# Kernel tuning notes

Measured on AMD Instinct MI355X. Metric: run time of the kernel, lower is better.

Reference implementation:

```python
import jax, jax.numpy as jnp
import numpy as np

N, D, C = 16384, 1024, 1024
EPS = 1e-6       # F.pairwise_distance eps added to the difference
DENOM_EPS = 1e-5


def setup_inputs() -> dict:
    key = jax.random.key(0)
    k1, k2, k3 = jax.random.split(key, 3)
    features = jax.random.normal(k1, (N, D), dtype=jnp.float32)
    labels = jax.random.randint(k2, (N,), 0, 10, dtype=jnp.int64)
    centers = jax.random.normal(k3, (C, D), dtype=jnp.float32)
    return {"features": features, "labels": labels, "centers": centers}


def reference(features, labels, centers):
    # torch: dist = ||f - c + eps||_2 per (sample, center) pair.
    # Expand exactly: ||f - c + eps||^2 = ||f||^2 + ||c||^2 - 2 f.c
    #                 + 2*eps*(sum(f) - sum(c)) + eps^2 * D
    f2 = jnp.sum(features * features, axis=1)            # [N]
    c2 = jnp.sum(centers * centers, axis=1)              # [C]
    fc = features @ centers.T                            # [N, C]
    fs = jnp.sum(features, axis=1)                       # [N]
    cs = jnp.sum(centers, axis=1)                        # [C]
    d = features.shape[1]
    sq = (f2[:, None] + c2[None, :] - 2.0 * fc
          + 2.0 * EPS * (fs[:, None] - cs[None, :]) + (EPS * EPS) * d)
    dist = jnp.sqrt(jnp.maximum(sq, 0.0))                # [N, C]
    min_dist = jnp.min(dist, axis=1)                     # [N]
    mask = (labels == 0).astype(min_dist.dtype)          # select label==0 samples
    count = jnp.sum(mask)
    loss = jnp.sum(min_dist * mask) / (count + DENOM_EPS)
    return loss
```

## Files before the change

### kernel.cpp

```cpp
#include <hip/hip_runtime.h>


constexpr int N = 16384;
constexpr int D = 1024;
constexpr int C = 1024;
constexpr float EPS = 1e-6f;

constexpr int SB = 16;
constexpr int CB = 128;
constexpr int BK = 64;
constexpr int NKT = D / BK;
constexpr int TPB = 256;
constexpr int DIST_GRID = 1024;

typedef __attribute__((ext_vector_type(8))) short bf16x8;
typedef __attribute__((ext_vector_type(4))) float f32x4;

__device__ inline unsigned mapf(float f) {
  unsigned b = __float_as_uint(f);
  return (b & 0x80000000u) ? ~b : (b | 0x80000000u);
}
__device__ inline float unmapf(unsigned u) {
  return __uint_as_float((u & 0x80000000u) ? (u ^ 0x80000000u) : ~u);
}

__device__ inline unsigned short f2bf(float x) {
  unsigned u = __float_as_uint(x);
  return (unsigned short)((u + 0x7FFFu + ((u >> 16) & 1u)) >> 16);
}

#define GLOAD_LDS16(gp, lp)                                        \
  __builtin_amdgcn_global_load_lds(                                \
      (const __attribute__((address_space(1))) void*)(gp),         \
      (__attribute__((address_space(3))) void*)(lp), 16, 0, 0)

__global__ __launch_bounds__(TPB) void k_setup(
    const float* __restrict__ feat, const int* __restrict__ labels,
    const float* __restrict__ cent, unsigned* __restrict__ count,
    unsigned* __restrict__ sel, unsigned* __restrict__ minmapped,
    float* __restrict__ cc, float* __restrict__ ff,
    unsigned short* __restrict__ cent_bf) {
  __shared__ float red[8];
  __shared__ unsigned lrow[16], lslot[16];
  __shared__ int lcount;

  const int b = blockIdx.x, t = threadIdx.x;
  const int lane = t & 63, w = t >> 6;

  if (t == 0) lcount = 0;
  __syncthreads();

  if (t < 16) {
    int n = b * 16 + t;
    minmapped[n] = 0xFFFFFFFFu;
    if (labels[n] == 0) {
      unsigned slot = atomicAdd(count, 1u);
      sel[slot] = (unsigned)n;
      int li = atomicAdd(&lcount, 1);
      lrow[li] = (unsigned)n;
      lslot[li] = slot;
    }
  }

  {
    const float* row = cent + (size_t)b * D;
    float4 v = *(const float4*)(row + t * 4);
    *(short4*)(cent_bf + (size_t)b * D + t * 4) =
        make_short4((short)f2bf(v.x), (short)f2bf(v.y), (short)f2bf(v.z),
                    (short)f2bf(v.w));
    float s1 = v.x + v.y + v.z + v.w;
    float s2 = v.x * v.x + v.y * v.y + v.z * v.z + v.w * v.w;
#pragma unroll
    for (int off = 32; off; off >>= 1) {
      s1 += __shfl_down(s1, off);
      s2 += __shfl_down(s2, off);
    }
    if (lane == 0) { red[w] = s1; red[4 + w] = s2; }
    __syncthreads();
    if (t == 0) {
      float a1 = red[0] + red[1] + red[2] + red[3];
      float a2 = red[4] + red[5] + red[6] + red[7];
      cc[b] = a2 - 2.0f * EPS * a1;
    }
  }

  const int nl = lcount;
  for (int i = 0; i < nl; ++i) {
    __syncthreads();
    const float* row = feat + (size_t)lrow[i] * D;
    float4 v = *(const float4*)(row + t * 4);
    float s1 = v.x + v.y + v.z + v.w;
    float s2 = v.x * v.x + v.y * v.y + v.z * v.z + v.w * v.w;
#pragma unroll
    for (int off = 32; off; off >>= 1) {
      s1 += __shfl_down(s1, off);
      s2 += __shfl_down(s2, off);
    }
    if (lane == 0) { red[w] = s1; red[4 + w] = s2; }
    __syncthreads();
    if (t == 0) {
      float a1 = red[0] + red[1] + red[2] + red[3];
      float a2 = red[4] + red[5] + red[6] + red[7];
      ff[lslot[i]] = a2 + 2.0f * EPS * a1 + EPS * EPS * (float)D;
    }
  }
}

__global__ __launch_bounds__(TPB) void k_dist(
    const float* __restrict__ feat, const unsigned short* __restrict__ cent_bf,
    const float* __restrict__ cc, const unsigned* __restrict__ count,
    const unsigned* __restrict__ sel, unsigned* __restrict__ minmapped,
    const float* __restrict__ ff, unsigned* __restrict__ done,
    float* __restrict__ out) {
  __shared__ __align__(16) unsigned short Cb[2][CB * BK];
  __shared__ __align__(16) unsigned short Fb[2][SB * BK];
  __shared__ unsigned rows_s[SB];
  __shared__ float red[4];
  __shared__ unsigned amlast;

  const unsigned cnt = *count;
  const unsigned nwork = ((cnt + SB - 1) / SB) * (C / CB);

  const int t = threadIdx.x;
  const int lane = t & 63, w = t >> 6;

  const int fs_ = t >> 4;
  const int fk4 = (t & 15) * 4;
  const int fj = fk4 >> 3, fhalf = (fk4 >> 2) & 1;
  const int foff = fs_ * BK + ((fj ^ (fs_ & 7)) << 3) + (fhalf << 2);
  const int arow = lane & 15, kg = lane >> 4;
  const int c0 = w * 32 + (lane & 15), c1 = c0 + 16;

  for (unsigned wk = blockIdx.x; wk < nwork; wk += DIST_GRID) {
    const unsigned sbase = (wk >> 3) * SB;
    const unsigned cbase = (wk & 7) * CB;

    if (t < SB) rows_s[t] = sel[min(sbase + (unsigned)t, cnt - 1u)];
    __syncthreads();

    const float* fsrc = feat + (size_t)rows_s[fs_] * D + fk4;
    f32x4 acc0 = {0.f, 0.f, 0.f, 0.f}, acc1 = {0.f, 0.f, 0.f, 0.f};

    auto stage = [&](int kt, int bb) {
      const int kbase = kt * BK;
#pragma unroll
      for (int u = 0; u < 4; ++u) {
        int chunk = (w * 4 + u) * 64 + lane;
        int r = chunk >> 3, j = chunk & 7;
        int jsrc = j ^ (r & 7);
        const unsigned short* src =
            cent_bf + (size_t)(cbase + r) * D + kbase + jsrc * 8;
        GLOAD_LDS16(src, &Cb[bb][chunk * 8]);
      }
      float4 v = *(const float4*)(fsrc + kbase);
      *(short4*)&Fb[bb][foff] = make_short4((short)f2bf(v.x), (short)f2bf(v.y),
                                            (short)f2bf(v.z), (short)f2bf(v.w));
    };

    stage(0, 0);
    __syncthreads();

    for (int kt = 0; kt < NKT; ++kt) {
      const int cur = kt & 1;
      if (kt + 1 < NKT) stage(kt + 1, cur ^ 1);
#pragma unroll
      for (int ks = 0; ks < 2; ++ks) {
        int jj = (ks << 2) + kg;
        bf16x8 a =
            *(const bf16x8*)&Fb[cur][arow * BK + ((jj ^ (arow & 7)) << 3)];
        bf16x8 b0 =
            *(const bf16x8*)&Cb[cur][c0 * BK + ((jj ^ (c0 & 7)) << 3)];
        bf16x8 b1 =
            *(const bf16x8*)&Cb[cur][c1 * BK + ((jj ^ (c1 & 7)) << 3)];
        acc0 = __builtin_amdgcn_mfma_f32_16x16x32_bf16(a, b0, acc0, 0, 0, 0);
        acc1 = __builtin_amdgcn_mfma_f32_16x16x32_bf16(a, b1, acc1, 0, 0, 0);
      }
      __syncthreads();
    }

    float ccv0 = cc[cbase + c0];
    float ccv1 = cc[cbase + c1];
#pragma unroll
    for (int reg = 0; reg < 4; ++reg) {
      float v = fminf(ccv0 - 2.0f * acc0[reg], ccv1 - 2.0f * acc1[reg]);
#pragma unroll
      for (int off = 1; off < 16; off <<= 1) v = fminf(v, __shfl_xor(v, off));
      if ((lane & 15) == 0) {
        unsigned sidx = sbase + (unsigned)((lane >> 4) * 4 + reg);
        if (sidx < cnt) atomicMin(&minmapped[sidx], mapf(v));
      }
    }
    __syncthreads();
  }

  if (t == 0) {
    __threadfence();
    amlast = (atomicAdd(done, 1u) == (unsigned)gridDim.x - 1u) ? 1u : 0u;
  }
  __syncthreads();
  if (amlast) {
    float s = 0.f;
    for (unsigned i = (unsigned)t; i < cnt; i += TPB) {
      float sq = ff[i] + unmapf(atomicAdd(&minmapped[i], 0u));
      s += sqrtf(fmaxf(sq, 0.0f));
    }
#pragma unroll
    for (int off = 32; off; off >>= 1) s += __shfl_down(s, off);
    if (lane == 0) red[w] = s;
    __syncthreads();
    if (t == 0) {
      float total = red[0] + red[1] + red[2] + red[3];
      out[0] = total / ((float)cnt + 1e-5f);
    }
  }
}

extern "C" void kernel_launch(void* const* d_in, const int* in_sizes, int n_in,
                              void* d_out, int out_size, void* d_ws, size_t ws_size,
                              hipStream_t stream) {
  const float* feat = (const float*)d_in[0];
  const int* labels = (const int*)d_in[1];
  const float* cent = (const float*)d_in[2];
  float* out = (float*)d_out;

  char* ws = (char*)d_ws;
  unsigned* count = (unsigned*)ws;
  unsigned* done = (unsigned*)(ws + 8);
  unsigned* minmapped = (unsigned*)(ws + 16);
  unsigned* sel = (unsigned*)(ws + 16 + 4 * (size_t)N);
  float* cc = (float*)(ws + 16 + 8 * (size_t)N);
  float* ff = (float*)(ws + 16 + 8 * (size_t)N + 4 * (size_t)C);
  unsigned short* cent_bf =
      (unsigned short*)(ws + 16 + 12 * (size_t)N + 4 * (size_t)C);

  hipMemsetAsync(d_ws, 0, 16, stream);

  k_setup<<<1024, TPB, 0, stream>>>(feat, labels, cent, count, sel, minmapped,
                                    cc, ff, cent_bf);
  k_dist<<<DIST_GRID, TPB, 0, stream>>>(feat, cent_bf, cc, count, sel,
                                        minmapped, ff, done, out);
}
```

Before: 156.6 us.

## Pre-convert selected features to bf16 and stream centers directly from global

The setup kernel now writes a compacted bf16 copy of the selected feature rows, so the distance kernel no longer gathers fp32 rows and converts them on every tile. The distance kernel loads the whole 16xD feature block into LDS once per work item with async global-to-LDS copies and a swizzled layout. It then reads center fragments straight from global memory into registers, with no LDS staging or per-k-tile barriers. The cost is losing LDS sharing and double buffering for the centers, and the inner loop now depends on global/L2 latency for the B operand.

```diff
diff --git a/kernel.cpp b/kernel.cpp
--- a/kernel.cpp
+++ b/kernel.cpp
@@ -8,8 +8,7 @@
 
 constexpr int SB = 16;
 constexpr int CB = 128;
-constexpr int BK = 64;
-constexpr int NKT = D / BK;
+constexpr int NSPLIT = C / CB;
 constexpr int TPB = 256;
 constexpr int DIST_GRID = 1024;
 
@@ -37,8 +36,8 @@
 __global__ __launch_bounds__(TPB) void k_setup(
     const float* __restrict__ feat, const int* __restrict__ labels,
     const float* __restrict__ cent, unsigned* __restrict__ count,
-    unsigned* __restrict__ sel, unsigned* __restrict__ minmapped,
-    float* __restrict__ cc, float* __restrict__ ff,
+    unsigned* __restrict__ minmapped, float* __restrict__ cc,
+    float* __restrict__ ff, unsigned short* __restrict__ fsel_bf,
     unsigned short* __restrict__ cent_bf) {
   __shared__ float red[8];
   __shared__ unsigned lrow[16], lslot[16];
@@ -55,7 +54,6 @@
     minmapped[n] = 0xFFFFFFFFu;
     if (labels[n] == 0) {
       unsigned slot = atomicAdd(count, 1u);
-      sel[slot] = (unsigned)n;
       int li = atomicAdd(&lcount, 1);
       lrow[li] = (unsigned)n;
       lslot[li] = slot;
@@ -89,6 +87,9 @@
     __syncthreads();
     const float* row = feat + (size_t)lrow[i] * D;
     float4 v = *(const float4*)(row + t * 4);
+    *(short4*)(fsel_bf + (size_t)lslot[i] * D + t * 4) =
+        make_short4((short)f2bf(v.x), (short)f2bf(v.y), (short)f2bf(v.z),
+                    (short)f2bf(v.w));
     float s1 = v.x + v.y + v.z + v.w;
     float s2 = v.x * v.x + v.y * v.y + v.z * v.z + v.w * v.w;
 #pragma unroll
@@ -107,79 +108,53 @@
 }
 
 __global__ __launch_bounds__(TPB) void k_dist(
-    const float* __restrict__ feat, const unsigned short* __restrict__ cent_bf,
-    const float* __restrict__ cc, const unsigned* __restrict__ count,
-    const unsigned* __restrict__ sel, unsigned* __restrict__ minmapped,
+    const unsigned short* __restrict__ fsel_bf,
+    const unsigned short* __restrict__ cent_bf, const float* __restrict__ cc,
+    const unsigned* __restrict__ count, unsigned* __restrict__ minmapped,
     const float* __restrict__ ff, unsigned* __restrict__ done,
     float* __restrict__ out) {
-  __shared__ __align__(16) unsigned short Cb[2][CB * BK];
-  __shared__ __align__(16) unsigned short Fb[2][SB * BK];
-  __shared__ unsigned rows_s[SB];
-  __shared__ float red[4];
-  __shared__ unsigned amlast;
+  __shared__ __align__(16) unsigned short Fb[SB * D];
 
   const unsigned cnt = *count;
-  const unsigned nwork = ((cnt + SB - 1) / SB) * (C / CB);
+  const unsigned nwork = ((cnt + SB - 1) / SB) * NSPLIT;
 
   const int t = threadIdx.x;
   const int lane = t & 63, w = t >> 6;
-
-  const int fs_ = t >> 4;
-  const int fk4 = (t & 15) * 4;
-  const int fj = fk4 >> 3, fhalf = (fk4 >> 2) & 1;
-  const int foff = fs_ * BK + ((fj ^ (fs_ & 7)) << 3) + (fhalf << 2);
   const int arow = lane & 15, kg = lane >> 4;
-  const int c0 = w * 32 + (lane & 15), c1 = c0 + 16;
+  const int c0 = w * 32 + (lane & 15);
+  const int fbase = arow * 128;
 
   for (unsigned wk = blockIdx.x; wk < nwork; wk += DIST_GRID) {
     const unsigned sbase = (wk >> 3) * SB;
     const unsigned cbase = (wk & 7) * CB;
 
-    if (t < SB) rows_s[t] = sel[min(sbase + (unsigned)t, cnt - 1u)];
-    __syncthreads();
-
-    const float* fsrc = feat + (size_t)rows_s[fs_] * D + fk4;
+#pragma unroll
+    for (int u = 0; u < 8; ++u) {
+      int chunk = u * 256 + t;
+      int r = chunk >> 7, j = chunk & 127;
+      int jsrc = (j & 0x78) | ((j ^ r) & 7);
+      unsigned srow = min(sbase + (unsigned)r, cnt - 1u);
+      GLOAD_LDS16(fsel_bf + (size_t)srow * D + jsrc * 8, &Fb[chunk * 8]);
+    }
+    __syncthreads();
+
+    const unsigned short* cp0 = cent_bf + (size_t)(cbase + c0) * D + kg * 8;
+    const unsigned short* cp1 = cp0 + (size_t)16 * D;
+
     f32x4 acc0 = {0.f, 0.f, 0.f, 0.f}, acc1 = {0.f, 0.f, 0.f, 0.f};
-
-    auto stage = [&](int kt, int bb) {
-      const int kbase = kt * BK;
-#pragma unroll
-      for (int u = 0; u < 4; ++u) {
-        int chunk = (w * 4 + u) * 64 + lane;
-        int r = chunk >> 3, j = chunk & 7;
-        int jsrc = j ^ (r & 7);
-        const unsigned short* src =
-            cent_bf + (size_t)(cbase + r) * D + kbase + jsrc * 8;
-        GLOAD_LDS16(src, &Cb[bb][chunk * 8]);
-      }
-      float4 v = *(const float4*)(fsrc + kbase);
-      *(short4*)&Fb[bb][foff] = make_short4((short)f2bf(v.x), (short)f2bf(v.y),
-                                            (short)f2bf(v.z), (short)f2bf(v.w));
-    };
-
-    stage(0, 0);
-    __syncthreads();
-
-    for (int kt = 0; kt < NKT; ++kt) {
-      const int cur = kt & 1;
-      if (kt + 1 < NKT) stage(kt + 1, cur ^ 1);
-#pragma unroll
-      for (int ks = 0; ks < 2; ++ks) {
-        int jj = (ks << 2) + kg;
-        bf16x8 a =
-            *(const bf16x8*)&Fb[cur][arow * BK + ((jj ^ (arow & 7)) << 3)];
-        bf16x8 b0 =
-            *(const bf16x8*)&Cb[cur][c0 * BK + ((jj ^ (c0 & 7)) << 3)];
-        bf16x8 b1 =
-            *(const bf16x8*)&Cb[cur][c1 * BK + ((jj ^ (c1 & 7)) << 3)];
-        acc0 = __builtin_amdgcn_mfma_f32_16x16x32_bf16(a, b0, acc0, 0, 0, 0);
-        acc1 = __builtin_amdgcn_mfma_f32_16x16x32_bf16(a, b1, acc1, 0, 0, 0);
-      }
-      __syncthreads();
+#pragma unroll 4
+    for (int ks = 0; ks < 32; ++ks) {
+      int cj = ks * 4 + kg;
+      int scj = (cj & 0x78) | ((cj ^ arow) & 7);
+      bf16x8 a = *(const bf16x8*)&Fb[(fbase + scj) * 8];
+      bf16x8 b0 = *(const bf16x8*)(cp0 + ks * 32);
+      bf16x8 b1 = *(const bf16x8*)(cp1 + ks * 32);
+      acc0 = __builtin_amdgcn_mfma_f32_16x16x32_bf16(a, b0, acc0, 0, 0, 0);
+      acc1 = __builtin_amdgcn_mfma_f32_16x16x32_bf16(a, b1, acc1, 0, 0, 0);
     }
 
     float ccv0 = cc[cbase + c0];
-    float ccv1 = cc[cbase + c1];
+    float ccv1 = cc[cbase + c0 + 16];
 #pragma unroll
     for (int reg = 0; reg < 4; ++reg) {
       float v = fminf(ccv0 - 2.0f * acc0[reg], ccv1 - 2.0f * acc1[reg]);
@@ -193,12 +168,14 @@
     __syncthreads();
   }
 
+  unsigned* flag = (unsigned*)Fb;
+  float* red = (float*)Fb + 1;
   if (t == 0) {
     __threadfence();
-    amlast = (atomicAdd(done, 1u) == (unsigned)gridDim.x - 1u) ? 1u : 0u;
+    flag[0] = (atomicAdd(done, 1u) == (unsigned)gridDim.x - 1u) ? 1u : 0u;
   }
   __syncthreads();
-  if (amlast) {
+  if (flag[0]) {
     float s = 0.f;
     for (unsigned i = (unsigned)t; i < cnt; i += TPB) {
       float sq = ff[i] + unmapf(atomicAdd(&minmapped[i], 0u));
@@ -227,16 +204,16 @@
   unsigned* count = (unsigned*)ws;
   unsigned* done = (unsigned*)(ws + 8);
   unsigned* minmapped = (unsigned*)(ws + 16);
-  unsigned* sel = (unsigned*)(ws + 16 + 4 * (size_t)N);
-  float* cc = (float*)(ws + 16 + 8 * (size_t)N);
-  float* ff = (float*)(ws + 16 + 8 * (size_t)N + 4 * (size_t)C);
-  unsigned short* cent_bf =
-      (unsigned short*)(ws + 16 + 12 * (size_t)N + 4 * (size_t)C);
+  float* cc = (float*)(ws + 16 + 4 * (size_t)N);
+  float* ff = (float*)(ws + 16 + 4 * (size_t)N + 4 * (size_t)C);
+  unsigned short* fsel_bf =
+      (unsigned short*)(ws + 16 + 8 * (size_t)N + 4 * (size_t)C);
+  unsigned short* cent_bf = fsel_bf + (size_t)N * D;
 
   hipMemsetAsync(d_ws, 0, 16, stream);
 
-  k_setup<<<1024, TPB, 0, stream>>>(feat, labels, cent, count, sel, minmapped,
-                                    cc, ff, cent_bf);
-  k_dist<<<DIST_GRID, TPB, 0, stream>>>(feat, cent_bf, cc, count, sel,
-                                        minmapped, ff, done, out);
-}
+  k_setup<<<1024, TPB, 0, stream>>>(feat, labels, cent, count, minmapped, cc,
+                                    ff, fsel_bf, cent_bf);
+  k_dist<<<DIST_GRID, TPB, 0, stream>>>(fsel_bf, cent_bf, cc, count, minmapped,
+                                        ff, done, out);
+}
```

Result: slower. 164.2 us (+4.8%).
